# Performance work log

Hardware: AMD Instinct MI355X
Metric: run time of the kernel (lower is better)

The kernel has to match this reference:

```python
import jax, jax.numpy as jnp
import numpy as np

T, H, E, I, K = 4096, 2048, 8, 1408, 2


def setup_inputs() -> dict:
    key = jax.random.key(0)
    k1, k2, k3, k4 = jax.random.split(key, 4)
    x = jax.random.normal(k1, (T, H), dtype=jnp.float32)
    router_w = jax.random.normal(k2, (H, E), dtype=jnp.float32) * 0.02
    gate_up_proj = jax.random.normal(k3, (E, H, 2 * I), dtype=jnp.float32) * 0.02
    down_proj = jax.random.normal(k4, (E, I, H), dtype=jnp.float32) * 0.02
    return {"x": x, "router_w": router_w, "gate_up_proj": gate_up_proj, "down_proj": down_proj}


def _moe_forward(x, router_w, gate_up_proj, down_proj):
    # --- Router: softmax over experts, top-k selection (Qwen2-MoE style) ---
    logits = x @ router_w                                  # [T, E]
    probs = jax.nn.softmax(logits, axis=-1)
    topk_w, topk_idx = jax.lax.top_k(probs, K)             # [T, K]

    # --- Permute: replicate tokens per selected expert, stable-sort by expert id ---
    flat_eid = topk_idx.reshape(-1)                        # [T*K]
    rep_x = jnp.repeat(x, K, axis=0)                       # [T*K, H]
    sort_idx = jnp.argsort(flat_eid, stable=True)          # token permute (like ops.permute)
    perm_x = rep_x[sort_idx]                               # [T*K, H] grouped by expert
    perm_eid = flat_eid[sort_idx]                          # [T*K]

    # --- Grouped expert MLP (gate_up GEMM -> SiLU*up -> down GEMM) ---
    # Faithful to grouped-GEMM math; expressed as a fixed loop over E experts
    # with row masking to stay jit-compatible (no data-dependent shapes).
    out = jnp.zeros_like(perm_x)
    for e in range(E):
        gu = perm_x @ gate_up_proj[e]                      # [T*K, 2I]
        gate, up = gu[:, :I], gu[:, I:]
        h = (jax.nn.silu(gate) * up) @ down_proj[e]        # [T*K, H]
        out = out + jnp.where((perm_eid == e)[:, None], h, 0.0)

    # --- Unpermute + weighted combine over top-k ---
    inv_sort = jnp.argsort(sort_idx)                       # inverse permute mapping
    unperm = out[inv_sort].reshape(T, K, H)
    return jnp.einsum('tkh,tk->th', unperm, topk_w)        # [T, H]


def reference(x, router_w, gate_up_proj, down_proj):
    return _moe_forward(x, router_w, gate_up_proj, down_proj)
```

## Files before the change

### kernel.cpp

```cpp
#include <hip/hip_runtime.h>
#include <hip/hip_bf16.h>

#define T_TOK 4096
#define H_DIM 2048
#define E_NUM 8
#define I_DIM 1408
#define RTOT  8192

typedef __bf16 bf16x8 __attribute__((ext_vector_type(8)));
typedef float  floatx4 __attribute__((ext_vector_type(4)));

__device__ __forceinline__ unsigned short f2bf(float f) {
  union { float f; unsigned u; } v; v.f = f;
  unsigned r = v.u + 0x7FFFu + ((v.u >> 16) & 1u);
  return (unsigned short)(r >> 16);
}

__device__ __forceinline__ void async16(const void* g, void* l) {
  __builtin_amdgcn_global_load_lds(
      (__attribute__((address_space(1))) void*)(g),
      (__attribute__((address_space(3))) void*)(l), 16, 0, 0);
}

__global__ void router_kernel(const float* __restrict__ x, const float* __restrict__ rw,
                              int* __restrict__ topk_idx, float* __restrict__ topk_w,
                              int* __restrict__ counts) {
  int wave = threadIdx.x >> 6, lane = threadIdx.x & 63;
  int t = blockIdx.x * 4 + wave;
  const float* xr = x + (size_t)t * H_DIM;
  float acc[E_NUM];
#pragma unroll
  for (int e = 0; e < E_NUM; e++) acc[e] = 0.f;
  for (int h = lane; h < H_DIM; h += 64) {
    float xv = xr[h];
    const float* wr = rw + h * E_NUM;
#pragma unroll
    for (int e = 0; e < E_NUM; e++) acc[e] += xv * wr[e];
  }
#pragma unroll
  for (int e = 0; e < E_NUM; e++) {
    float v = acc[e];
#pragma unroll
    for (int s = 32; s > 0; s >>= 1) v += __shfl_xor(v, s, 64);
    acc[e] = v;
  }
  if (lane == 0) {
    float mx = acc[0];
#pragma unroll
    for (int e = 1; e < E_NUM; e++) mx = fmaxf(mx, acc[e]);
    float p[E_NUM], s = 0.f;
#pragma unroll
    for (int e = 0; e < E_NUM; e++) { p[e] = __expf(acc[e] - mx); s += p[e]; }
    float inv = 1.0f / s;
    int i0 = 0;
#pragma unroll
    for (int e = 1; e < E_NUM; e++) if (p[e] > p[i0]) i0 = e;
    int i1 = (i0 == 0) ? 1 : 0;
#pragma unroll
    for (int e = 0; e < E_NUM; e++) if (e != i0 && p[e] > p[i1]) i1 = e;
    topk_idx[t * 2]     = i0;
    topk_idx[t * 2 + 1] = i1;
    topk_w[t * 2]       = p[i0] * inv;
    topk_w[t * 2 + 1]   = p[i1] * inv;
    atomicAdd(&counts[i0], 1);
    atomicAdd(&counts[i1], 1);
  }
}

__global__ void scan_kernel(const int* __restrict__ counts, int* __restrict__ offsets,
                            int* __restrict__ cursors) {
  if (threadIdx.x == 0) {
    int o = 0;
    for (int e = 0; e < E_NUM; e++) { offsets[e] = o; cursors[e] = o; o += counts[e]; }
  }
}

__global__ void assign_kernel(const int* __restrict__ topk_idx, int* __restrict__ cursors,
                              int* __restrict__ row_of, int* __restrict__ tok_of) {
  int i = blockIdx.x * blockDim.x + threadIdx.x;
  int e = topk_idx[i];
  int row = atomicAdd(&cursors[e], 1);
  row_of[i] = row;
  tok_of[row] = i >> 1;
}

__global__ void gather_kernel(const float* __restrict__ x, const int* __restrict__ tok_of,
                              unsigned short* __restrict__ Xp) {
  int row = blockIdx.x;
  int t = tok_of[row];
  const float4* src = (const float4*)(x + (size_t)t * H_DIM);
  ushort4* dst = (ushort4*)(Xp + (size_t)row * H_DIM);
  for (int i = threadIdx.x; i < H_DIM / 4; i += 256) {
    float4 v = src[i];
    ushort4 o;
    o.x = f2bf(v.x); o.y = f2bf(v.y); o.z = f2bf(v.z); o.w = f2bf(v.w);
    dst[i] = o;
  }
}

__global__ void convert_gu_kernel(const float* __restrict__ W,
                                  unsigned short* __restrict__ WgT,
                                  unsigned short* __restrict__ WuT) {
  __shared__ float tile[32][33];
  int e = blockIdx.z;
  int k0 = blockIdx.y * 32;
  int n0 = blockIdx.x * 32;
  const float* Wp = W + (size_t)e * H_DIM * (2 * I_DIM);
  int tx = threadIdx.x & 31, ty = threadIdx.x >> 5;
#pragma unroll
  for (int i = 0; i < 4; i++) {
    int k = ty + i * 8;
    tile[k][tx] = Wp[(size_t)(k0 + k) * (2 * I_DIM) + n0 + tx];
  }
  __syncthreads();
  unsigned short* Op;
  int nb = n0;
  if (n0 < I_DIM) Op = WgT + (size_t)e * I_DIM * H_DIM;
  else { Op = WuT + (size_t)e * I_DIM * H_DIM; nb = n0 - I_DIM; }
#pragma unroll
  for (int i = 0; i < 4; i++) {
    int n = ty + i * 8;
    Op[(size_t)(nb + n) * H_DIM + k0 + tx] = f2bf(tile[tx][n]);
  }
}

__global__ void convert_dn_kernel(const float* __restrict__ W,
                                  unsigned short* __restrict__ WdT) {
  __shared__ float tile[32][33];
  int e = blockIdx.z;
  int k0 = blockIdx.y * 32;
  int n0 = blockIdx.x * 32;
  const float* Wp = W + (size_t)e * I_DIM * H_DIM;
  int tx = threadIdx.x & 31, ty = threadIdx.x >> 5;
#pragma unroll
  for (int i = 0; i < 4; i++) {
    int k = ty + i * 8;
    tile[k][tx] = Wp[(size_t)(k0 + k) * H_DIM + n0 + tx];
  }
  __syncthreads();
  unsigned short* Op = WdT + (size_t)e * H_DIM * I_DIM;
#pragma unroll
  for (int i = 0; i < 4; i++) {
    int n = ty + i * 8;
    Op[(size_t)(n0 + n) * I_DIM + k0 + tx] = f2bf(tile[tx][n]);
  }
}

__global__ __launch_bounds__(256, 2) void gemm1_kernel(
    const unsigned short* __restrict__ Xp,
    const unsigned short* __restrict__ WgT,
    const unsigned short* __restrict__ WuT,
    const int* __restrict__ offsets, const int* __restrict__ counts,
    unsigned short* __restrict__ Hmid) {
  int e = blockIdx.z;
  int cnt = counts[e];
  if ((int)blockIdx.y * 128 >= cnt) return;
  int row_beg = offsets[e];
  int m0 = row_beg + blockIdx.y * 128;
  int row_end = row_beg + cnt;
  int n0 = blockIdx.x * 128;

  __shared__ unsigned short sA[128 * 32];
  __shared__ unsigned short sBg[128 * 32];
  __shared__ unsigned short sBu[128 * 32];

  int tid = threadIdx.x;
  int wave = tid >> 6, lane = tid & 63;

  const unsigned short* ga[2];
  const unsigned short* ggt[2];
  const unsigned short* gut[2];
  unsigned short *la[2], *lg[2], *lu[2];
  const size_t wbase = (size_t)e * I_DIM * H_DIM;
#pragma unroll
  for (int r = 0; r < 2; r++) {
    int lin = r * 256 + tid;
    int row = lin >> 2;
    int col = (lin & 3) * 8;
    int am = m0 + row; if (am > RTOT - 1) am = RTOT - 1;
    ga[r]  = Xp  + (size_t)am * H_DIM + col;
    ggt[r] = WgT + wbase + (size_t)(n0 + row) * H_DIM + col;
    gut[r] = WuT + wbase + (size_t)(n0 + row) * H_DIM + col;
    la[r] = sA  + lin * 8;
    lg[r] = sBg + lin * 8;
    lu[r] = sBu + lin * 8;
  }

  floatx4 accg[4][4] = {};
  floatx4 accu[4][4] = {};

  const unsigned short* sAb = sA  + ((wave & 1) * 64 + (lane & 15)) * 32 + (lane >> 4) * 8;
  const unsigned short* sGb = sBg + ((wave >> 1) * 64 + (lane & 15)) * 32 + (lane >> 4) * 8;
  const unsigned short* sUb = sBu + ((wave >> 1) * 64 + (lane & 15)) * 32 + (lane >> 4) * 8;

  for (int kb = 0; kb < H_DIM / 32; kb++) {
    __syncthreads();
#pragma unroll
    for (int r = 0; r < 2; r++) {
      async16(ga[r],  la[r]); ga[r]  += 32;
      async16(ggt[r], lg[r]); ggt[r] += 32;
      async16(gut[r], lu[r]); gut[r] += 32;
    }
    __syncthreads();
    bf16x8 a[4];
#pragma unroll
    for (int mi = 0; mi < 4; mi++) a[mi] = *(const bf16x8*)(sAb + mi * 16 * 32);
#pragma unroll
    for (int ni = 0; ni < 4; ni++) {
      bf16x8 bg = *(const bf16x8*)(sGb + ni * 16 * 32);
      bf16x8 bu = *(const bf16x8*)(sUb + ni * 16 * 32);
#pragma unroll
      for (int mi = 0; mi < 4; mi++) {
        accg[mi][ni] = __builtin_amdgcn_mfma_f32_16x16x32_bf16(a[mi], bg, accg[mi][ni], 0, 0, 0);
        accu[mi][ni] = __builtin_amdgcn_mfma_f32_16x16x32_bf16(a[mi], bu, accu[mi][ni], 0, 0, 0);
      }
    }
  }

  int mrow = m0 + (wave & 1) * 64 + (lane >> 4) * 4;
  int ncol = n0 + (wave >> 1) * 64 + (lane & 15);
#pragma unroll
  for (int mi = 0; mi < 4; mi++) {
#pragma unroll
    for (int r = 0; r < 4; r++) {
      int m = mrow + mi * 16 + r;
      if (m < row_end) {
        size_t base = (size_t)m * I_DIM + ncol;
#pragma unroll
        for (int ni = 0; ni < 4; ni++) {
          float g = accg[mi][ni][r];
          float u = accu[mi][ni][r];
          float s = g / (1.0f + __expf(-g));
          Hmid[base + ni * 16] = f2bf(s * u);
        }
      }
    }
  }
}

__global__ __launch_bounds__(256, 2) void gemm2_kernel(
    const unsigned short* __restrict__ Hmid,
    const unsigned short* __restrict__ WdT,
    const int* __restrict__ offsets, const int* __restrict__ counts,
    float* __restrict__ H2) {
  int e = blockIdx.z;
  int cnt = counts[e];
  if ((int)blockIdx.y * 128 >= cnt) return;
  int row_beg = offsets[e];
  int m0 = row_beg + blockIdx.y * 128;
  int row_end = row_beg + cnt;
  int n0 = blockIdx.x * 128;

  __shared__ unsigned short sA[128 * 32];
  __shared__ unsigned short sB[128 * 32];

  int tid = threadIdx.x;
  int wave = tid >> 6, lane = tid & 63;

  const unsigned short* ga[2];
  const unsigned short* gb[2];
  unsigned short *la[2], *lb[2];
  const size_t wbase = (size_t)e * H_DIM * I_DIM;
#pragma unroll
  for (int r = 0; r < 2; r++) {
    int lin = r * 256 + tid;
    int row = lin >> 2;
    int col = (lin & 3) * 8;
    int am = m0 + row; if (am > RTOT - 1) am = RTOT - 1;
    ga[r] = Hmid + (size_t)am * I_DIM + col;
    gb[r] = WdT + wbase + (size_t)(n0 + row) * I_DIM + col;
    la[r] = sA + lin * 8;
    lb[r] = sB + lin * 8;
  }

  floatx4 acc[4][4] = {};

  const unsigned short* sAb = sA + ((wave & 1) * 64 + (lane & 15)) * 32 + (lane >> 4) * 8;
  const unsigned short* sBb = sB + ((wave >> 1) * 64 + (lane & 15)) * 32 + (lane >> 4) * 8;

  for (int kb = 0; kb < I_DIM / 32; kb++) {
    __syncthreads();
#pragma unroll
    for (int r = 0; r < 2; r++) {
      async16(ga[r], la[r]); ga[r] += 32;
      async16(gb[r], lb[r]); gb[r] += 32;
    }
    __syncthreads();
    bf16x8 a[4];
#pragma unroll
    for (int mi = 0; mi < 4; mi++) a[mi] = *(const bf16x8*)(sAb + mi * 16 * 32);
#pragma unroll
    for (int ni = 0; ni < 4; ni++) {
      bf16x8 b = *(const bf16x8*)(sBb + ni * 16 * 32);
#pragma unroll
      for (int mi = 0; mi < 4; mi++)
        acc[mi][ni] = __builtin_amdgcn_mfma_f32_16x16x32_bf16(a[mi], b, acc[mi][ni], 0, 0, 0);
    }
  }

  int mrow = m0 + (wave & 1) * 64 + (lane >> 4) * 4;
  int ncol = n0 + (wave >> 1) * 64 + (lane & 15);
#pragma unroll
  for (int mi = 0; mi < 4; mi++) {
#pragma unroll
    for (int r = 0; r < 4; r++) {
      int m = mrow + mi * 16 + r;
      if (m < row_end) {
        size_t base = (size_t)m * H_DIM + ncol;
#pragma unroll
        for (int ni = 0; ni < 4; ni++) H2[base + ni * 16] = acc[mi][ni][r];
      }
    }
  }
}

__global__ void combine_kernel(const float* __restrict__ H2, const int* __restrict__ row_of,
                               const float* __restrict__ topk_w, float* __restrict__ out) {
  int t = blockIdx.x >> 1;
  int part = blockIdx.x & 1;
  int c = part * 1024 + threadIdx.x * 4;
  int r0 = row_of[t * 2], r1 = row_of[t * 2 + 1];
  float w0 = topk_w[t * 2], w1 = topk_w[t * 2 + 1];
  float4 a = *(const float4*)(H2 + (size_t)r0 * H_DIM + c);
  float4 b = *(const float4*)(H2 + (size_t)r1 * H_DIM + c);
  float4 o;
  o.x = w0 * a.x + w1 * b.x;
  o.y = w0 * a.y + w1 * b.y;
  o.z = w0 * a.z + w1 * b.z;
  o.w = w0 * a.w + w1 * b.w;
  *(float4*)(out + (size_t)t * H_DIM + c) = o;
}

extern "C" void kernel_launch(void* const* d_in, const int* in_sizes, int n_in,
                              void* d_out, int out_size, void* d_ws, size_t ws_size,
                              hipStream_t stream) {
  const float* x   = (const float*)d_in[0];
  const float* rw  = (const float*)d_in[1];
  const float* wgu = (const float*)d_in[2];
  const float* wdn = (const float*)d_in[3];
  float* out = (float*)d_out;

  char* ws = (char*)d_ws;
  size_t off = 0;
  auto alloc = [&](size_t b) {
    char* p = ws + off;
    off = (off + b + 255) & ~(size_t)255;
    return p;
  };
  unsigned short* WgT  = (unsigned short*)alloc((size_t)E_NUM * I_DIM * H_DIM * 2);
  unsigned short* WuT  = (unsigned short*)alloc((size_t)E_NUM * I_DIM * H_DIM * 2);
  unsigned short* WdT  = (unsigned short*)alloc((size_t)E_NUM * H_DIM * I_DIM * 2);
  unsigned short* Xp   = (unsigned short*)alloc((size_t)RTOT * H_DIM * 2);
  unsigned short* Hmid = (unsigned short*)alloc((size_t)RTOT * I_DIM * 2);
  float* H2            = (float*)alloc((size_t)RTOT * H_DIM * 4);
  int*   topk_idx      = (int*)alloc(RTOT * 4);
  float* topk_w        = (float*)alloc(RTOT * 4);
  int*   row_of        = (int*)alloc(RTOT * 4);
  int*   tok_of        = (int*)alloc(RTOT * 4);
  int*   counts        = (int*)alloc(256);
  int*   offsets       = (int*)alloc(256);
  int*   cursors       = (int*)alloc(256);

  hipMemsetAsync(counts, 0, E_NUM * sizeof(int), stream);

  convert_gu_kernel<<<dim3(88, 64, 8), 256, 0, stream>>>(wgu, WgT, WuT);
  convert_dn_kernel<<<dim3(64, 44, 8), 256, 0, stream>>>(wdn, WdT);
  router_kernel<<<T_TOK / 4, 256, 0, stream>>>(x, rw, topk_idx, topk_w, counts);
  scan_kernel<<<1, 64, 0, stream>>>(counts, offsets, cursors);
  assign_kernel<<<RTOT / 256, 256, 0, stream>>>(topk_idx, cursors, row_of, tok_of);
  gather_kernel<<<RTOT, 256, 0, stream>>>(x, tok_of, Xp);
  gemm1_kernel<<<dim3(11, 64, 8), 256, 0, stream>>>(Xp, WgT, WuT, offsets, counts, Hmid);
  gemm2_kernel<<<dim3(16, 64, 8), 256, 0, stream>>>(Hmid, WdT, offsets, counts, H2);
  combine_kernel<<<T_TOK * 2, 256, 0, stream>>>(H2, row_of, topk_w, out);
}
```

Measured before the change: 801.5 us.

## Use compact tile list with XCD-aware scheduling and fuse combine into down GEMM

The scan kernel now builds a compact list of 128-row tiles across experts, up to 72 entries. Both GEMMs launch a 1D grid and map block IDs so that tiles sharing an XCD reuse weight panels, replacing the padded 3D grid in which most blocks exited early. The down GEMM applies the top-k weight and atomically adds results directly into the zeroed output. This removes the H2 intermediate buffer and the separate combine kernel, at the cost of float atomics and nondeterministic summation order.

```diff
diff --git a/kernel.cpp b/kernel.cpp
--- a/kernel.cpp
+++ b/kernel.cpp
@@ -6,6 +6,7 @@
 #define E_NUM 8
 #define I_DIM 1408
 #define RTOT  8192
+#define MAXTILES 72
 
 typedef __bf16 bf16x8 __attribute__((ext_vector_type(8)));
 typedef float  floatx4 __attribute__((ext_vector_type(4)));
@@ -68,20 +69,31 @@
 }
 
 __global__ void scan_kernel(const int* __restrict__ counts, int* __restrict__ offsets,
-                            int* __restrict__ cursors) {
+                            int* __restrict__ cursors, int* __restrict__ tile_e,
+                            int* __restrict__ tile_m0, int* __restrict__ tile_end) {
   if (threadIdx.x == 0) {
-    int o = 0;
-    for (int e = 0; e < E_NUM; e++) { offsets[e] = o; cursors[e] = o; o += counts[e]; }
-  }
-}
-
-__global__ void assign_kernel(const int* __restrict__ topk_idx, int* __restrict__ cursors,
-                              int* __restrict__ row_of, int* __restrict__ tok_of) {
+    int o = 0, nt = 0;
+    for (int e = 0; e < E_NUM; e++) {
+      offsets[e] = o; cursors[e] = o;
+      int c = counts[e];
+      for (int m = 0; m < c; m += 128) {
+        tile_e[nt] = e; tile_m0[nt] = o + m; tile_end[nt] = o + c; nt++;
+      }
+      o += c;
+    }
+    for (; nt < MAXTILES; nt++) tile_e[nt] = -1;
+  }
+}
+
+__global__ void assign_kernel(const int* __restrict__ topk_idx, const float* __restrict__ topk_w,
+                              int* __restrict__ cursors, int* __restrict__ row_of,
+                              int* __restrict__ tok_of, float* __restrict__ w_of) {
   int i = blockIdx.x * blockDim.x + threadIdx.x;
   int e = topk_idx[i];
   int row = atomicAdd(&cursors[e], 1);
   row_of[i] = row;
   tok_of[row] = i >> 1;
+  w_of[row] = topk_w[i];
 }
 
 __global__ void gather_kernel(const float* __restrict__ x, const int* __restrict__ tok_of,
@@ -150,15 +162,25 @@
     const unsigned short* __restrict__ Xp,
     const unsigned short* __restrict__ WgT,
     const unsigned short* __restrict__ WuT,
-    const int* __restrict__ offsets, const int* __restrict__ counts,
+    const int* __restrict__ tile_e, const int* __restrict__ tile_m0,
+    const int* __restrict__ tile_end,
     unsigned short* __restrict__ Hmid) {
-  int e = blockIdx.z;
-  int cnt = counts[e];
-  if ((int)blockIdx.y * 128 >= cnt) return;
-  int row_beg = offsets[e];
-  int m0 = row_beg + blockIdx.y * 128;
-  int row_end = row_beg + cnt;
-  int n0 = blockIdx.x * 128;
+  int bid = blockIdx.x;
+  int xcd = bid & 7, j = bid >> 3;
+  int mt, n;
+  if (j < 88) {
+    int c = j / 44, jj = j % 44;
+    n = jj >> 2;
+    mt = xcd * 9 + c * 4 + (jj & 3);
+  } else {
+    mt = xcd * 9 + 8;
+    n = j - 88;
+  }
+  int e = tile_e[mt];
+  if (e < 0) return;
+  int m0 = tile_m0[mt];
+  int row_end = tile_end[mt];
+  int n0 = n * 128;
 
   __shared__ unsigned short sA[128 * 32];
   __shared__ unsigned short sBg[128 * 32];
@@ -241,15 +263,26 @@
 __global__ __launch_bounds__(256, 2) void gemm2_kernel(
     const unsigned short* __restrict__ Hmid,
     const unsigned short* __restrict__ WdT,
-    const int* __restrict__ offsets, const int* __restrict__ counts,
-    float* __restrict__ H2) {
-  int e = blockIdx.z;
-  int cnt = counts[e];
-  if ((int)blockIdx.y * 128 >= cnt) return;
-  int row_beg = offsets[e];
-  int m0 = row_beg + blockIdx.y * 128;
-  int row_end = row_beg + cnt;
-  int n0 = blockIdx.x * 128;
+    const int* __restrict__ tile_e, const int* __restrict__ tile_m0,
+    const int* __restrict__ tile_end,
+    const int* __restrict__ tok_of, const float* __restrict__ w_of,
+    float* __restrict__ out) {
+  int bid = blockIdx.x;
+  int xcd = bid & 7, j = bid >> 3;
+  int mt, n;
+  if (j < 128) {
+    int c = j / 64, jj = j % 64;
+    n = jj >> 2;
+    mt = xcd * 9 + c * 4 + (jj & 3);
+  } else {
+    mt = xcd * 9 + 8;
+    n = j - 128;
+  }
+  int e = tile_e[mt];
+  if (e < 0) return;
+  int m0 = tile_m0[mt];
+  int row_end = tile_end[mt];
+  int n0 = n * 128;
 
   __shared__ unsigned short sA[128 * 32];
   __shared__ unsigned short sB[128 * 32];
@@ -306,29 +339,15 @@
     for (int r = 0; r < 4; r++) {
       int m = mrow + mi * 16 + r;
       if (m < row_end) {
-        size_t base = (size_t)m * H_DIM + ncol;
-#pragma unroll
-        for (int ni = 0; ni < 4; ni++) H2[base + ni * 16] = acc[mi][ni][r];
+        int t = tok_of[m];
+        float w = w_of[m];
+        float* op = out + (size_t)t * H_DIM + ncol;
+#pragma unroll
+        for (int ni = 0; ni < 4; ni++)
+          atomicAdd(op + ni * 16, w * acc[mi][ni][r]);
       }
     }
   }
-}
-
-__global__ void combine_kernel(const float* __restrict__ H2, const int* __restrict__ row_of,
-                               const float* __restrict__ topk_w, float* __restrict__ out) {
-  int t = blockIdx.x >> 1;
-  int part = blockIdx.x & 1;
-  int c = part * 1024 + threadIdx.x * 4;
-  int r0 = row_of[t * 2], r1 = row_of[t * 2 + 1];
-  float w0 = topk_w[t * 2], w1 = topk_w[t * 2 + 1];
-  float4 a = *(const float4*)(H2 + (size_t)r0 * H_DIM + c);
-  float4 b = *(const float4*)(H2 + (size_t)r1 * H_DIM + c);
-  float4 o;
-  o.x = w0 * a.x + w1 * b.x;
-  o.y = w0 * a.y + w1 * b.y;
-  o.z = w0 * a.z + w1 * b.z;
-  o.w = w0 * a.w + w1 * b.w;
-  *(float4*)(out + (size_t)t * H_DIM + c) = o;
 }
 
 extern "C" void kernel_launch(void* const* d_in, const int* in_sizes, int n_in,
@@ -352,24 +371,27 @@
   unsigned short* WdT  = (unsigned short*)alloc((size_t)E_NUM * H_DIM * I_DIM * 2);
   unsigned short* Xp   = (unsigned short*)alloc((size_t)RTOT * H_DIM * 2);
   unsigned short* Hmid = (unsigned short*)alloc((size_t)RTOT * I_DIM * 2);
-  float* H2            = (float*)alloc((size_t)RTOT * H_DIM * 4);
   int*   topk_idx      = (int*)alloc(RTOT * 4);
   float* topk_w        = (float*)alloc(RTOT * 4);
   int*   row_of        = (int*)alloc(RTOT * 4);
   int*   tok_of        = (int*)alloc(RTOT * 4);
+  float* w_of          = (float*)alloc(RTOT * 4);
   int*   counts        = (int*)alloc(256);
   int*   offsets       = (int*)alloc(256);
   int*   cursors       = (int*)alloc(256);
+  int*   tile_e        = (int*)alloc(128 * 4);
+  int*   tile_m0       = (int*)alloc(128 * 4);
+  int*   tile_end      = (int*)alloc(128 * 4);
 
   hipMemsetAsync(counts, 0, E_NUM * sizeof(int), stream);
+  hipMemsetAsync(d_out, 0, (size_t)out_size * sizeof(float), stream);
 
   convert_gu_kernel<<<dim3(88, 64, 8), 256, 0, stream>>>(wgu, WgT, WuT);
   convert_dn_kernel<<<dim3(64, 44, 8), 256, 0, stream>>>(wdn, WdT);
   router_kernel<<<T_TOK / 4, 256, 0, stream>>>(x, rw, topk_idx, topk_w, counts);
-  scan_kernel<<<1, 64, 0, stream>>>(counts, offsets, cursors);
-  assign_kernel<<<RTOT / 256, 256, 0, stream>>>(topk_idx, cursors, row_of, tok_of);
+  scan_kernel<<<1, 64, 0, stream>>>(counts, offsets, cursors, tile_e, tile_m0, tile_end);
+  assign_kernel<<<RTOT / 256, 256, 0, stream>>>(topk_idx, topk_w, cursors, row_of, tok_of, w_of);
   gather_kernel<<<RTOT, 256, 0, stream>>>(x, tok_of, Xp);
-  gemm1_kernel<<<dim3(11, 64, 8), 256, 0, stream>>>(Xp, WgT, WuT, offsets, counts, Hmid);
-  gemm2_kernel<<<dim3(16, 64, 8), 256, 0, stream>>>(Hmid, WdT, offsets, counts, H2);
-  combine_kernel<<<T_TOK * 2, 256, 0, stream>>>(H2, row_of, topk_w, out);
-}
+  gemm1_kernel<<<8 * 9 * 11, 256, 0, stream>>>(Xp, WgT, WuT, tile_e, tile_m0, tile_end, Hmid);
+  gemm2_kernel<<<8 * 9 * 16, 256, 0, stream>>>(Hmid, WdT, tile_e, tile_m0, tile_end, tok_of, w_of, out);
+}
```

New measurement: 789.1 us. About the same (-1.5%).
